# Performance work log

Measured on AMD Instinct MI355X. Metric: run time of the kernel, lower is better.

The kernel has to match this reference:

```python
import jax, jax.numpy as jnp
import numpy as np

DIM = 1024
HEADS = 8
HEAD_DIM = DIM // HEADS
FFN = 4096
B, N = 32, 1024
EPS = 1e-5


def layer_norm(x, g, b):
    mu = jnp.mean(x, axis=-1, keepdims=True)
    var = jnp.mean(jnp.square(x - mu), axis=-1, keepdims=True)
    return (x - mu) * jax.lax.rsqrt(var + EPS) * g + b


def setup_inputs() -> dict:
    key = jax.random.key(0)
    ks = jax.random.split(key, 10)
    s = 0.02
    return {
        "x": jax.random.normal(ks[0], (B, N, DIM), dtype=jnp.float32),
        "haltingscore": jnp.zeros((B, N), dtype=jnp.float32),
        "Wq": jax.random.normal(ks[1], (DIM, DIM), dtype=jnp.float32) * s,
        "Wkv": jax.random.normal(ks[2], (DIM, 2 * DIM), dtype=jnp.float32) * s,
        "Wp": jax.random.normal(ks[3], (DIM, DIM), dtype=jnp.float32) * s,
        "bp": jnp.zeros((DIM,), dtype=jnp.float32),
        "W1": jax.random.normal(ks[4], (DIM, FFN), dtype=jnp.float32) * s,
        "b1": jnp.zeros((FFN,), dtype=jnp.float32),
        "W2": jax.random.normal(ks[5], (FFN, DIM), dtype=jnp.float32) * s,
        "b2": jnp.zeros((DIM,), dtype=jnp.float32),
        "ln1_g": jnp.ones((DIM,), dtype=jnp.float32),
        "ln1_b": jnp.zeros((DIM,), dtype=jnp.float32),
        "ln2_g": jnp.ones((DIM,), dtype=jnp.float32),
        "ln2_b": jnp.zeros((DIM,), dtype=jnp.float32),
    }


def reference(x, haltingscore, Wq, Wkv, Wp, bp, W1, b1, W2, b2,
              ln1_g, ln1_b, ln2_g, ln2_b):
    b, n, c = x.shape
    scale = HEAD_DIM ** -0.5
    # ---- EfficientAttention (explicit QK^T softmax V) ----
    q = (x @ Wq).reshape(b, n, HEADS, HEAD_DIM).transpose(0, 2, 1, 3)  # bhnd
    kv = (x @ Wkv).reshape(b, n, 2, HEADS, HEAD_DIM).transpose(2, 0, 3, 1, 4)
    k, v = kv[0], kv[1]                                               # bhnd
    attn = jax.nn.softmax(jnp.einsum('bhnd,bhmd->bhnm', q, k) * scale, axis=-1)
    o = jnp.einsum('bhnm,bhmd->bhnd', attn, v)
    o = o.transpose(0, 2, 1, 3).reshape(b, n, c)
    o = o @ Wp + bp
    attn_mean = jnp.mean(attn, axis=1)                                # (B, N, N)
    # ---- residual + LN1 ----
    h = layer_norm(x + o, ln1_g, ln1_b)
    # ---- FFN + residual + LN2 ----
    ff = jax.nn.relu(h @ W1 + b1) @ W2 + b2
    out = layer_norm(h + ff, ln2_g, ln2_b)
    # ---- halting score update ----
    a = jax.nn.softmax(jnp.sum(attn_mean, axis=1), axis=-1)           # (B, N)
    halting = haltingscore + a
    return (out, halting, a)
```

## Files before the change

### kernel.cpp

```cpp
#include <hip/hip_runtime.h>
#include <hip/hip_bf16.h>
#include <stdint.h>

#define DIMC 1024
#define HEADS 8
#define HDIM 128
#define FFND 4096
#define BATCH 32
#define SEQ 1024
#define SROWS (BATCH*SEQ)
#define QSTR 3072

typedef unsigned short u16;
typedef short short4v __attribute__((ext_vector_type(4)));
typedef short short8 __attribute__((ext_vector_type(8)));
typedef float f32x4 __attribute__((ext_vector_type(4)));
typedef __bf16 bf16x8 __attribute__((ext_vector_type(8)));

__device__ __forceinline__ u16 f2bf(float f) {
    union { float f; uint32_t u; } x{f};
    uint32_t r = x.u + 0x7FFFu + ((x.u >> 16) & 1u);
    return (u16)(r >> 16);
}
__device__ __forceinline__ float bf2f(u16 h) {
    union { uint32_t u; float f; } x;
    x.u = ((uint32_t)h) << 16;
    return x.f;
}

__device__ __forceinline__ f32x4 mfma16(short8 a, short8 b, f32x4 c) {
    return __builtin_amdgcn_mfma_f32_16x16x32_bf16(
        __builtin_bit_cast(bf16x8, a), __builtin_bit_cast(bf16x8, b), c, 0, 0, 0);
}

__device__ __forceinline__ void gload_lds16(const u16* g, u16* lds) {
    __builtin_amdgcn_global_load_lds(
        (const __attribute__((address_space(1))) uint32_t*)g,
        (__attribute__((address_space(3))) uint32_t*)lds, 16, 0, 0);
}

__global__ __launch_bounds__(256) void k_cast(const float* __restrict__ in,
                                              u16* __restrict__ out, int n4) {
    int i = blockIdx.x * 256 + threadIdx.x;
    if (i < n4) {
        f32x4 v = ((const f32x4*)in)[i];
        uint32_t lo = f2bf(v[0]) | ((uint32_t)f2bf(v[1]) << 16);
        uint32_t hi = f2bf(v[2]) | ((uint32_t)f2bf(v[3]) << 16);
        ((uint2*)out)[i] = make_uint2(lo, hi);
    }
}

__global__ __launch_bounds__(256) void k_transpose_cast(const float* __restrict__ W,
                                                        u16* __restrict__ Wt,
                                                        int K, int N) {
    __shared__ u16 tile[32][33];
    int n0 = blockIdx.x * 32, k0 = blockIdx.y * 32;
    int tx = threadIdx.x, ty = threadIdx.y;
#pragma unroll
    for (int i = 0; i < 32; i += 8)
        tile[ty + i][tx] = f2bf(W[(size_t)(k0 + ty + i) * N + n0 + tx]);
    __syncthreads();
#pragma unroll
    for (int i = 0; i < 32; i += 8)
        Wt[(size_t)(n0 + ty + i) * K + k0 + tx] = tile[tx][ty + i];
}

template<bool OUT_BF16, bool RELU, bool BIAS, bool VSPLIT>
__global__ __launch_bounds__(512, 2) void k_gemm256(const u16* __restrict__ A,
                                                    const u16* __restrict__ Bt,
                                                    const float* __restrict__ bias,
                                                    void* __restrict__ C,
                                                    u16* __restrict__ Vt,
                                                    int M, int N, int K) {
    union Smem {
        struct { u16 A[4][8192]; u16 B[4][8192]; } k;
        u16 ob[64 * 264];
        float of[64 * 268];
        u16 vt[256 * 66];
    };
    __shared__ Smem smem;
    const int tid = threadIdx.x;
    const int lane = tid & 63, wv = tid >> 6;
    const int wm = wv >> 2, wn = wv & 3;
    const int l15 = lane & 15, lg = lane >> 4;
    const int gx = gridDim.x;
    const int nwg = gx * gridDim.y;
    const int id = blockIdx.y * gx + blockIdx.x;
    const int id2 = (id & 7) * (nwg >> 3) + (id >> 3);
    const int row0 = (id2 / gx) << 8, col0 = (id2 % gx) << 8;
    const int NT = K >> 5;

#define STAGE_A(tt) {                                                          \
    int _t = (tt);                                                             \
    _Pragma("unroll")                                                          \
    for (int i = 0; i < 2; ++i) {                                              \
        int blk = wv * 2 + i;                                                  \
        gload_lds16(A + (size_t)(row0 + blk * 16 + l15) * K + _t * 32 + lg * 8,\
                    &smem.k.A[_t & 3][blk * 512]);                             \
    } }
#define STAGE_B(tt) {                                                          \
    int _t = (tt);                                                             \
    _Pragma("unroll")                                                          \
    for (int i = 0; i < 2; ++i) {                                              \
        int blk = wv * 2 + i;                                                  \
        gload_lds16(Bt + (size_t)(col0 + blk * 16 + l15) * K + _t * 32 + lg * 8,\
                    &smem.k.B[_t & 3][blk * 512]);                             \
    } }

    STAGE_A(0); STAGE_B(0);
    STAGE_A(1); STAGE_B(1);
    STAGE_A(2); STAGE_B(2);

    f32x4 acc[8][4] = {};
    for (int t = 0; t < NT; ++t) {
        const int slot = t & 3;
        if (t <= NT - 3)      asm volatile("s_waitcnt vmcnt(8)" ::: "memory");
        else if (t == NT - 2) asm volatile("s_waitcnt vmcnt(4)" ::: "memory");
        else                  asm volatile("s_waitcnt vmcnt(0)" ::: "memory");
        __builtin_amdgcn_s_barrier();
        __builtin_amdgcn_sched_barrier(0);

        const u16* Ab = &smem.k.A[slot][(wm * 8) * 512];
        const u16* Bb = &smem.k.B[slot][(wn * 4) * 512];

        if (t + 3 < NT) STAGE_A(t + 3);
        short8 bf[4], af[4];
#pragma unroll
        for (int n = 0; n < 4; ++n) bf[n] = *(const short8*)(Bb + n * 512 + lane * 8);
#pragma unroll
        for (int m = 0; m < 4; ++m) af[m] = *(const short8*)(Ab + m * 512 + lane * 8);
        __builtin_amdgcn_s_setprio(1);
#pragma unroll
        for (int m = 0; m < 4; ++m)
#pragma unroll
            for (int n = 0; n < 4; ++n)
                acc[m][n] = mfma16(af[m], bf[n], acc[m][n]);
        __builtin_amdgcn_s_setprio(0);

        if (t + 3 < NT) STAGE_B(t + 3);
#pragma unroll
        for (int m = 0; m < 4; ++m) af[m] = *(const short8*)(Ab + (4 + m) * 512 + lane * 8);
        __builtin_amdgcn_s_setprio(1);
#pragma unroll
        for (int m = 0; m < 4; ++m)
#pragma unroll
            for (int n = 0; n < 4; ++n)
                acc[4 + m][n] = mfma16(af[m], bf[n], acc[4 + m][n]);
        __builtin_amdgcn_s_setprio(0);
    }
#undef STAGE_A
#undef STAGE_B

    const bool vpath = VSPLIT && (col0 >= 2048);
    __syncthreads();
#pragma unroll
    for (int s = 0; s < 4; ++s) {
        if (s) __syncthreads();
        if (wm == (s >> 1)) {
            const int mb4 = (s & 1) * 4;
#pragma unroll
            for (int mm = 0; mm < 4; ++mm)
#pragma unroll
                for (int n = 0; n < 4; ++n) {
                    int c = wn * 64 + n * 16 + l15;
                    float bv = BIAS ? bias[col0 + c] : 0.f;
#pragma unroll
                    for (int j = 0; j < 4; ++j) {
                        int lr = mm * 16 + lg * 4 + j;
                        float v = acc[mb4 + mm][n][j] + bv;
                        if (RELU) v = fmaxf(v, 0.f);
                        if (vpath)         smem.vt[c * 66 + lr] = f2bf(v);
                        else if (OUT_BF16) smem.ob[lr * 264 + c] = f2bf(v);
                        else               smem.of[lr * 268 + c] = v;
                    }
                }
        }
        __syncthreads();
        const int gr0 = row0 + s * 64;
        if (vpath) {
            const int bb = gr0 >> 10;
            const int mb = gr0 & 1023;
#pragma unroll
            for (int it = 0; it < 4; ++it) {
                int idx = it * 512 + tid;
                int dc = idx >> 3, mseg = idx & 7;
                int hh = (col0 - 2048 + dc) >> 7;
                int dd = (col0 - 2048 + dc) & 127;
                *(short8*)(Vt + ((size_t)(bb * 8 + hh)) * (HDIM * SEQ)
                              + (size_t)dd * SEQ + mb + mseg * 8) =
                    *(const short8*)(&smem.vt[dc * 66 + mseg * 8]);
            }
        } else if (OUT_BF16) {
#pragma unroll
            for (int it = 0; it < 4; ++it) {
                int idx = it * 512 + tid;
                int r = idx >> 5, seg = idx & 31;
                *(short8*)((u16*)C + (size_t)(gr0 + r) * N + col0 + seg * 8) =
                    *(const short8*)(&smem.ob[r * 264 + seg * 8]);
            }
        } else {
#pragma unroll
            for (int it = 0; it < 8; ++it) {
                int idx = it * 512 + tid;
                int r = idx >> 6, seg = idx & 63;
                *(f32x4*)((float*)C + (size_t)(gr0 + r) * N + col0 + seg * 4) =
                    *(const f32x4*)(&smem.of[r * 268 + seg * 4]);
            }
        }
    }
}

__global__ __launch_bounds__(256, 3) void k_attn(const u16* __restrict__ QKV,
                                                 const u16* __restrict__ Vt,
                                                 u16* __restrict__ O,
                                                 float* __restrict__ csp) {
    __shared__ u16 Kl[2][4096];
    __shared__ u16 Vl[2][4096];
    __shared__ u16 p_lds[4][1280];
    __shared__ float cs[1024];
    const int id = blockIdx.x;
    const int id2 = (id & 7) * 256 + (id >> 3);
    const int qt = id2 & 7, bh = id2 >> 3;
    const int b = bh >> 3, h = bh & 7;
    const int tid = threadIdx.x, lane = tid & 63, wv = tid >> 6;
    const int l15 = lane & 15, lg = lane >> 4;

    for (int i = tid; i < 1024; i += 256) cs[i] = 0.f;

    const int q0 = qt * 128 + wv * 32;
    const u16* qbaseA = QKV + (size_t)(b * SEQ + q0 + l15) * QSTR + h * HDIM + lg * 8;
    const u16* qbaseB = qbaseA + (size_t)16 * QSTR;
    short8 qfA[4], qfB[4];
#pragma unroll
    for (int kk = 0; kk < 4; ++kk) {
        qfA[kk] = *(const short8*)(qbaseA + kk * 32);
        qfB[kk] = *(const short8*)(qbaseB + kk * 32);
    }
    const float CEXP = 0.12751743f;
    const u16* kbase = QKV + (size_t)(b * SEQ) * QSTR + 1024 + h * HDIM;
    const u16* vtb = Vt + (size_t)bh * HDIM * SEQ;

#define STAGE_K(tt) { _Pragma("unroll")                                         \
    for (int i = 0; i < 2; ++i) { int c = wv * 2 + i;                           \
        gload_lds16(kbase + (size_t)((tt) * 32 + (c >> 2) * 16 + l15) * QSTR    \
                    + (c & 3) * 32 + lg * 8, &Kl[(tt) & 1][c * 512]); } }
#define STAGE_V(tt) { _Pragma("unroll")                                         \
    for (int i = 0; i < 2; ++i) { int c = wv * 2 + i;                           \
        gload_lds16(vtb + (size_t)(c * 16 + l15) * SEQ + (tt) * 32 + lg * 8,    \
                    &Vl[(tt) & 1][c * 512]); } }

    STAGE_K(0);
    asm volatile("s_waitcnt vmcnt(0)" ::: "memory");
    __builtin_amdgcn_s_barrier();
    f32x4 rsA = {0.f, 0.f, 0.f, 0.f}, rsB = {0.f, 0.f, 0.f, 0.f};
    for (int t = 0; t < 32; ++t) {
        if (t < 31) STAGE_K(t + 1);
        const u16* Kp = &Kl[t & 1][0];
        f32x4 sA0 = {0.f,0.f,0.f,0.f}, sA1 = {0.f,0.f,0.f,0.f};
        f32x4 sB0 = {0.f,0.f,0.f,0.f}, sB1 = {0.f,0.f,0.f,0.f};
        __builtin_amdgcn_s_setprio(1);
#pragma unroll
        for (int kk = 0; kk < 4; ++kk) {
            short8 b0 = *(const short8*)(Kp + kk * 512 + lane * 8);
            short8 b1 = *(const short8*)(Kp + (4 + kk) * 512 + lane * 8);
            sA0 = mfma16(qfA[kk], b0, sA0);
            sA1 = mfma16(qfA[kk], b1, sA1);
            sB0 = mfma16(qfB[kk], b0, sB0);
            sB1 = mfma16(qfB[kk], b1, sB1);
        }
        __builtin_amdgcn_s_setprio(0);
#pragma unroll
        for (int r = 0; r < 4; ++r) {
            rsA[r] += __builtin_amdgcn_exp2f(sA0[r] * CEXP)
                    + __builtin_amdgcn_exp2f(sA1[r] * CEXP);
            rsB[r] += __builtin_amdgcn_exp2f(sB0[r] * CEXP)
                    + __builtin_amdgcn_exp2f(sB1[r] * CEXP);
        }
        asm volatile("s_waitcnt vmcnt(0)" ::: "memory");
        __builtin_amdgcn_s_barrier();
    }
#pragma unroll
    for (int o = 1; o < 16; o <<= 1)
#pragma unroll
        for (int r = 0; r < 4; ++r) {
            rsA[r] += __shfl_xor(rsA[r], o);
            rsB[r] += __shfl_xor(rsB[r], o);
        }
    f32x4 inv_rsA, inv_rsB;
#pragma unroll
    for (int r = 0; r < 4; ++r) {
        inv_rsA[r] = 1.f / rsA[r];
        inv_rsB[r] = 1.f / rsB[r];
    }

    STAGE_K(0); STAGE_V(0);
    asm volatile("s_waitcnt vmcnt(0)" ::: "memory");
    __builtin_amdgcn_s_barrier();
    f32x4 odA[8] = {}, odB[8] = {};
    u16* pl = &p_lds[wv][0];
    for (int t = 0; t < 32; ++t) {
        const int m0 = t * 32;
        if (t < 31) { STAGE_K(t + 1); STAGE_V(t + 1); }
        const u16* Kp = &Kl[t & 1][0];
        f32x4 sA0 = {0.f,0.f,0.f,0.f}, sA1 = {0.f,0.f,0.f,0.f};
        f32x4 sB0 = {0.f,0.f,0.f,0.f}, sB1 = {0.f,0.f,0.f,0.f};
        __builtin_amdgcn_s_setprio(1);
#pragma unroll
        for (int kk = 0; kk < 4; ++kk) {
            short8 b0 = *(const short8*)(Kp + kk * 512 + lane * 8);
            short8 b1 = *(const short8*)(Kp + (4 + kk) * 512 + lane * 8);
            sA0 = mfma16(qfA[kk], b0, sA0);
            sA1 = mfma16(qfA[kk], b1, sA1);
            sB0 = mfma16(qfB[kk], b0, sB0);
            sB1 = mfma16(qfB[kk], b1, sB1);
        }
        __builtin_amdgcn_s_setprio(0);
        float pA0[4], pA1[4], pB0[4], pB1[4];
#pragma unroll
        for (int r = 0; r < 4; ++r) {
            pA0[r] = __builtin_amdgcn_exp2f(sA0[r] * CEXP) * inv_rsA[r];
            pA1[r] = __builtin_amdgcn_exp2f(sA1[r] * CEXP) * inv_rsA[r];
            pB0[r] = __builtin_amdgcn_exp2f(sB0[r] * CEXP) * inv_rsB[r];
            pB1[r] = __builtin_amdgcn_exp2f(sB1[r] * CEXP) * inv_rsB[r];
        }
        float c0 = pA0[0] + pA0[1] + pA0[2] + pA0[3]
                 + pB0[0] + pB0[1] + pB0[2] + pB0[3];
        float c1 = pA1[0] + pA1[1] + pA1[2] + pA1[3]
                 + pB1[0] + pB1[1] + pB1[2] + pB1[3];
        c0 += __shfl_xor(c0, 16); c0 += __shfl_xor(c0, 32);
        c1 += __shfl_xor(c1, 16); c1 += __shfl_xor(c1, 32);
        if (lane < 16)      atomicAdd(&cs[m0 + lane], c0);
        else if (lane < 32) atomicAdd(&cs[m0 + lane], c1);
#pragma unroll
        for (int r = 0; r < 4; ++r) {
            pl[(lg * 4 + r) * 40 + l15]           = f2bf(pA0[r]);
            pl[(lg * 4 + r) * 40 + 16 + l15]      = f2bf(pA1[r]);
            pl[(16 + lg * 4 + r) * 40 + l15]      = f2bf(pB0[r]);
            pl[(16 + lg * 4 + r) * 40 + 16 + l15] = f2bf(pB1[r]);
        }
        short8 paA = *(const short8*)(pl + l15 * 40 + lg * 8);
        short8 paB = *(const short8*)(pl + (16 + l15) * 40 + lg * 8);
        const u16* Vb_ = &Vl[t & 1][0];
        __builtin_amdgcn_s_setprio(1);
#pragma unroll
        for (int db = 0; db < 8; ++db) {
            short8 vf = *(const short8*)(Vb_ + db * 512 + lane * 8);
            odA[db] = mfma16(paA, vf, odA[db]);
            odB[db] = mfma16(paB, vf, odB[db]);
        }
        __builtin_amdgcn_s_setprio(0);
        asm volatile("s_waitcnt vmcnt(0)" ::: "memory");
        __builtin_amdgcn_s_barrier();
    }
#undef STAGE_K
#undef STAGE_V
    __syncthreads();
    u16* obA = O + (size_t)(b * SEQ + q0 + lg * 4) * DIMC + h * HDIM + l15;
    u16* obB = obA + (size_t)16 * DIMC;
#pragma unroll
    for (int db = 0; db < 8; ++db)
#pragma unroll
        for (int r = 0; r < 4; ++r) {
            obA[(size_t)r * DIMC + db * 16] = f2bf(odA[db][r]);
            obB[(size_t)r * DIMC + db * 16] = f2bf(odB[db][r]);
        }
    for (int m = tid; m < 1024; m += 256)
        csp[((size_t)bh * 8 + qt) * 1024 + m] = cs[m];
}

__global__ __launch_bounds__(256) void k_ln1(const float* __restrict__ xa,
                                             const u16* __restrict__ pj,
                                             const float* __restrict__ g,
                                             const float* __restrict__ bt,
                                             u16* __restrict__ ob) {
    const int row = blockIdx.x;
    const int t = threadIdx.x, lane = t & 63, wv = t >> 6;
    f32x4 va = ((const f32x4*)(xa + (size_t)row * DIMC))[t];
    short4v hv = ((const short4v*)(pj + (size_t)row * DIMC))[t];
    f32x4 s;
#pragma unroll
    for (int j = 0; j < 4; ++j) s[j] = va[j] + bf2f((u16)hv[j]);
    float sum = s[0] + s[1] + s[2] + s[3];
    float sq = s[0]*s[0] + s[1]*s[1] + s[2]*s[2] + s[3]*s[3];
#pragma unroll
    for (int o = 1; o < 64; o <<= 1) { sum += __shfl_xor(sum, o); sq += __shfl_xor(sq, o); }
    __shared__ float red[8];
    if (lane == 0) { red[wv] = sum; red[4 + wv] = sq; }
    __syncthreads();
    sum = red[0] + red[1] + red[2] + red[3];
    sq  = red[4] + red[5] + red[6] + red[7];
    float mu = sum * (1.f / DIMC);
    float rstd = rsqrtf(sq * (1.f / DIMC) - mu * mu + 1e-5f);
    f32x4 gg = ((const f32x4*)g)[t];
    f32x4 bb = ((const f32x4*)bt)[t];
    uint32_t lo, hi;
    float o0 = (s[0] - mu) * rstd * gg[0] + bb[0];
    float o1 = (s[1] - mu) * rstd * gg[1] + bb[1];
    float o2 = (s[2] - mu) * rstd * gg[2] + bb[2];
    float o3 = (s[3] - mu) * rstd * gg[3] + bb[3];
    lo = f2bf(o0) | ((uint32_t)f2bf(o1) << 16);
    hi = f2bf(o2) | ((uint32_t)f2bf(o3) << 16);
    ((uint2*)(ob + (size_t)row * DIMC))[t] = make_uint2(lo, hi);
}

__global__ __launch_bounds__(256) void k_ln2(const u16* __restrict__ xa,
                                             const u16* __restrict__ f2,
                                             const float* __restrict__ g,
                                             const float* __restrict__ bt,
                                             float* __restrict__ of) {
    const int row = blockIdx.x;
    const int t = threadIdx.x, lane = t & 63, wv = t >> 6;
    short4v hv = ((const short4v*)(xa + (size_t)row * DIMC))[t];
    short4v fv = ((const short4v*)(f2 + (size_t)row * DIMC))[t];
    f32x4 s;
#pragma unroll
    for (int j = 0; j < 4; ++j) s[j] = bf2f((u16)hv[j]) + bf2f((u16)fv[j]);
    float sum = s[0] + s[1] + s[2] + s[3];
    float sq = s[0]*s[0] + s[1]*s[1] + s[2]*s[2] + s[3]*s[3];
#pragma unroll
    for (int o = 1; o < 64; o <<= 1) { sum += __shfl_xor(sum, o); sq += __shfl_xor(sq, o); }
    __shared__ float red[8];
    if (lane == 0) { red[wv] = sum; red[4 + wv] = sq; }
    __syncthreads();
    sum = red[0] + red[1] + red[2] + red[3];
    sq  = red[4] + red[5] + red[6] + red[7];
    float mu = sum * (1.f / DIMC);
    float rstd = rsqrtf(sq * (1.f / DIMC) - mu * mu + 1e-5f);
    f32x4 gg = ((const f32x4*)g)[t];
    f32x4 bb = ((const f32x4*)bt)[t];
    f32x4 o4;
#pragma unroll
    for (int j = 0; j < 4; ++j) o4[j] = (s[j] - mu) * rstd * gg[j] + bb[j];
    ((f32x4*)(of + (size_t)row * DIMC))[t] = o4;
}

__global__ __launch_bounds__(256) void k_halt(const float* __restrict__ csp,
                                              const float* __restrict__ hs,
                                              float* __restrict__ halt_out,
                                              float* __restrict__ a_out) {
    const int b = blockIdx.x, t = threadIdx.x, lane = t & 63, wv = t >> 6;
    const float* base = csp + (size_t)b * 65536;
    float acc[4] = {0.f, 0.f, 0.f, 0.f};
    for (int s2 = 0; s2 < 64; ++s2) {
#pragma unroll
        for (int j = 0; j < 4; ++j) acc[j] += base[(size_t)s2 * 1024 + j * 256 + t];
    }
    float mx = -1e30f;
#pragma unroll
    for (int j = 0; j < 4; ++j) { acc[j] *= 0.125f; mx = fmaxf(mx, acc[j]); }
#pragma unroll
    for (int o = 1; o < 64; o <<= 1) mx = fmaxf(mx, __shfl_xor(mx, o));
    __shared__ float red[8];
    if (lane == 0) red[wv] = mx;
    __syncthreads();
    mx = fmaxf(fmaxf(red[0], red[1]), fmaxf(red[2], red[3]));
    float e[4]; float sum = 0.f;
#pragma unroll
    for (int j = 0; j < 4; ++j) { e[j] = __expf(acc[j] - mx); sum += e[j]; }
#pragma unroll
    for (int o = 1; o < 64; o <<= 1) sum += __shfl_xor(sum, o);
    if (lane == 0) red[4 + wv] = sum;
    __syncthreads();
    sum = red[4] + red[5] + red[6] + red[7];
    float inv = 1.f / sum;
#pragma unroll
    for (int j = 0; j < 4; ++j) {
        int m = j * 256 + t;
        float a = e[j] * inv;
        a_out[b * SEQ + m] = a;
        halt_out[b * SEQ + m] = hs[b * SEQ + m] + a;
    }
}

extern "C" void kernel_launch(void* const* d_in, const int* in_sizes, int n_in,
                              void* d_out, int out_size, void* d_ws, size_t ws_size,
                              hipStream_t stream) {
    (void)in_sizes; (void)n_in; (void)out_size; (void)ws_size;
    const float* x   = (const float*)d_in[0];
    const float* hs  = (const float*)d_in[1];
    const float* Wq  = (const float*)d_in[2];
    const float* Wkv = (const float*)d_in[3];
    const float* Wp  = (const float*)d_in[4];
    const float* bp  = (const float*)d_in[5];
    const float* W1  = (const float*)d_in[6];
    const float* b1  = (const float*)d_in[7];
    const float* W2  = (const float*)d_in[8];
    const float* b2  = (const float*)d_in[9];
    const float* g1  = (const float*)d_in[10];
    const float* be1 = (const float*)d_in[11];
    const float* g2  = (const float*)d_in[12];
    const float* be2 = (const float*)d_in[13];

    float* out = (float*)d_out;
    float* halt_out = out + (size_t)SROWS * DIMC;
    float* a_out = halt_out + SROWS;

    char* w = (char*)d_ws;
    const size_t MB = 1024 * 1024;
    u16*  xb    = (u16*)(w);
    u16*  qkv   = (u16*)(w + 64 * MB);
    u16*  Vt    = (u16*)(w + 256 * MB);
    u16*  WqkvT = (u16*)(w + 320 * MB);
    u16*  WpT   = (u16*)(w + 326 * MB);
    u16*  W1T   = (u16*)(w + 328 * MB);
    u16*  W2T   = (u16*)(w + 336 * MB);
    float* csp  = (float*)(w + 344 * MB);
    u16*  o_b   = (u16*)(w);
    u16*  projb = (u16*)(w + 64 * MB);
    u16*  hb    = (u16*)(w);
    u16*  ff1   = (u16*)(w + 64 * MB);
    u16*  ff2b  = (u16*)(w + 192 * MB);

    dim3 tb(32, 8);
    k_cast<<<SROWS * DIMC / 4 / 256, 256, 0, stream>>>(x, xb, SROWS * DIMC / 4);
    k_transpose_cast<<<dim3(DIMC / 32, DIMC / 32), tb, 0, stream>>>(Wq, WqkvT, DIMC, DIMC);
    k_transpose_cast<<<dim3(2 * DIMC / 32, DIMC / 32), tb, 0, stream>>>(
        Wkv, WqkvT + (size_t)DIMC * DIMC, DIMC, 2 * DIMC);
    k_transpose_cast<<<dim3(DIMC / 32, DIMC / 32), tb, 0, stream>>>(Wp, WpT, DIMC, DIMC);
    k_transpose_cast<<<dim3(FFND / 32, DIMC / 32), tb, 0, stream>>>(W1, W1T, DIMC, FFND);
    k_transpose_cast<<<dim3(DIMC / 32, FFND / 32), tb, 0, stream>>>(W2, W2T, FFND, DIMC);
    k_gemm256<true, false, false, true><<<dim3(QSTR / 256, SROWS / 256), 512, 0, stream>>>(
        xb, WqkvT, nullptr, qkv, Vt, SROWS, QSTR, DIMC);
    k_attn<<<2048, 256, 0, stream>>>(qkv, Vt, o_b, csp);
    k_gemm256<true, false, true, false><<<dim3(DIMC / 256, SROWS / 256), 512, 0, stream>>>(
        o_b, WpT, bp, projb, nullptr, SROWS, DIMC, DIMC);
    k_ln1<<<SROWS, 256, 0, stream>>>(x, projb, g1, be1, hb);
    for (int c = 0; c < 2; ++c) {
        const size_t ro = (size_t)c * 16384;
        k_gemm256<true, true, true, false><<<dim3(FFND / 256, 16384 / 256), 512, 0, stream>>>(
            hb + ro * DIMC, W1T, b1, ff1, nullptr, 16384, FFND, DIMC);
        k_gemm256<true, false, true, false><<<dim3(DIMC / 256, 16384 / 256), 512, 0, stream>>>(
            ff1, W2T, b2, ff2b, nullptr, 16384, DIMC, FFND);
        k_ln2<<<16384, 256, 0, stream>>>(hb + ro * DIMC, ff2b, g2, be2, out + ro * DIMC);
    }
    k_halt<<<BATCH, 256, 0, stream>>>(csp, hs, halt_out, a_out);
}
```

Baseline: 1.472 ms.

## Transpose QK MFMA operands and build P fragments in registers via cross-lane shuffles

Swaps the MFMA operand order so S^T is computed, giving each lane a column of scores. The P→bf16 fragment is then assembled in registers with v_cvt_pk_bf16_f32 and xor shuffles, removing the per-wave LDS round trip for P. Column sums for the attention mean now use DPP row-rotate reductions. The row-sum pass loads 64-key tiles through a union-shared LDS buffer, halving its barrier count. This trades LDS traffic and barriers for extra shuffle and select instructions, and the fragment-permutation correctness is delicate.

Result: no change. 1.445 ms (-1.8%).

```diff
diff --git a/kernel.cpp b/kernel.cpp
--- a/kernel.cpp
+++ b/kernel.cpp
@@ -37,6 +37,36 @@
     __builtin_amdgcn_global_load_lds(
         (const __attribute__((address_space(1))) uint32_t*)g,
         (__attribute__((address_space(3))) uint32_t*)lds, 16, 0, 0);
+}
+
+#define DPP_RORADD(x, ctrl) do {                                               \
+    int _t = __builtin_amdgcn_mov_dpp(__builtin_bit_cast(int, (x)), (ctrl),    \
+                                      0xf, 0xf, true);                         \
+    (x) += __builtin_bit_cast(float, _t); } while (0)
+
+__device__ __forceinline__ short8 p2frag(f32x4 p0, f32x4 p1, int lane) {
+    uint32_t a, b, c, d;
+    asm("v_cvt_pk_bf16_f32 %0, %1, %2" : "=v"(a) : "v"(p0[0]), "v"(p0[1]));
+    asm("v_cvt_pk_bf16_f32 %0, %1, %2" : "=v"(b) : "v"(p0[2]), "v"(p0[3]));
+    asm("v_cvt_pk_bf16_f32 %0, %1, %2" : "=v"(c) : "v"(p1[0]), "v"(p1[1]));
+    asm("v_cvt_pk_bf16_f32 %0, %1, %2" : "=v"(d) : "v"(p1[2]), "v"(p1[3]));
+    uint32_t ax = (uint32_t)__shfl_xor((int)a, 32);
+    uint32_t bx = (uint32_t)__shfl_xor((int)b, 32);
+    uint32_t cx = (uint32_t)__shfl_xor((int)c, 32);
+    uint32_t dx = (uint32_t)__shfl_xor((int)d, 32);
+    const bool up = (lane & 32) != 0;
+    uint32_t P = up ? cx : a, Q = up ? c : ax;
+    uint32_t R = up ? dx : b, S = up ? d : bx;
+    uint32_t Px = (uint32_t)__shfl_xor((int)P, 16);
+    uint32_t Qx = (uint32_t)__shfl_xor((int)Q, 16);
+    uint32_t Rx = (uint32_t)__shfl_xor((int)R, 16);
+    uint32_t Sx = (uint32_t)__shfl_xor((int)S, 16);
+    const bool odd = (lane & 16) != 0;
+    uint32_t w0 = odd ? Qx : P,  w1 = odd ? Sx : R;
+    uint32_t w2 = odd ? Q  : Px, w3 = odd ? S  : Rx;
+    union { uint32_t w[4]; short8 s; } u;
+    u.w[0] = w0; u.w[1] = w1; u.w[2] = w2; u.w[3] = w3;
+    return u.s;
 }
 
 __global__ __launch_bounds__(256) void k_cast(const float* __restrict__ in,
@@ -214,9 +244,11 @@
                                                  const u16* __restrict__ Vt,
                                                  u16* __restrict__ O,
                                                  float* __restrict__ csp) {
-    __shared__ u16 Kl[2][4096];
-    __shared__ u16 Vl[2][4096];
-    __shared__ u16 p_lds[4][1280];
+    union Sm {
+        u16 K2[2][8192];
+        struct { u16 Kl[2][4096]; u16 Vl[2][4096]; } pb;
+    };
+    __shared__ Sm sm;
     __shared__ float cs[1024];
     const int id = blockIdx.x;
     const int id2 = (id & 7) * 256 + (id >> 3);
@@ -240,107 +272,115 @@
     const u16* kbase = QKV + (size_t)(b * SEQ) * QSTR + 1024 + h * HDIM;
     const u16* vtb = Vt + (size_t)bh * HDIM * SEQ;
 
+#define STAGE_K2(tt) { _Pragma("unroll")                                        \
+    for (int i = 0; i < 4; ++i) {                                               \
+        gload_lds16(kbase + (size_t)((tt) * 64 + wv * 16 + l15) * QSTR          \
+                    + i * 32 + lg * 8, &sm.K2[(tt) & 1][(wv * 4 + i) * 512]); } }
 #define STAGE_K(tt) { _Pragma("unroll")                                         \
     for (int i = 0; i < 2; ++i) { int c = wv * 2 + i;                           \
         gload_lds16(kbase + (size_t)((tt) * 32 + (c >> 2) * 16 + l15) * QSTR    \
-                    + (c & 3) * 32 + lg * 8, &Kl[(tt) & 1][c * 512]); } }
+                    + (c & 3) * 32 + lg * 8, &sm.pb.Kl[(tt) & 1][c * 512]); } }
 #define STAGE_V(tt) { _Pragma("unroll")                                         \
     for (int i = 0; i < 2; ++i) { int c = wv * 2 + i;                           \
         gload_lds16(vtb + (size_t)(c * 16 + l15) * SEQ + (tt) * 32 + lg * 8,    \
-                    &Vl[(tt) & 1][c * 512]); } }
-
-    STAGE_K(0);
+                    &sm.pb.Vl[(tt) & 1][c * 512]); } }
+
+    STAGE_K2(0);
     asm volatile("s_waitcnt vmcnt(0)" ::: "memory");
     __builtin_amdgcn_s_barrier();
-    f32x4 rsA = {0.f, 0.f, 0.f, 0.f}, rsB = {0.f, 0.f, 0.f, 0.f};
-    for (int t = 0; t < 32; ++t) {
-        if (t < 31) STAGE_K(t + 1);
-        const u16* Kp = &Kl[t & 1][0];
-        f32x4 sA0 = {0.f,0.f,0.f,0.f}, sA1 = {0.f,0.f,0.f,0.f};
-        f32x4 sB0 = {0.f,0.f,0.f,0.f}, sB1 = {0.f,0.f,0.f,0.f};
+    f32x4 rsA4 = {0.f, 0.f, 0.f, 0.f}, rsB4 = {0.f, 0.f, 0.f, 0.f};
+    for (int t = 0; t < 16; ++t) {
+        if (t < 15) STAGE_K2(t + 1);
+        const u16* Kp = &sm.K2[t & 1][0];
         __builtin_amdgcn_s_setprio(1);
 #pragma unroll
-        for (int kk = 0; kk < 4; ++kk) {
-            short8 b0 = *(const short8*)(Kp + kk * 512 + lane * 8);
-            short8 b1 = *(const short8*)(Kp + (4 + kk) * 512 + lane * 8);
-            sA0 = mfma16(qfA[kk], b0, sA0);
-            sA1 = mfma16(qfA[kk], b1, sA1);
-            sB0 = mfma16(qfB[kk], b0, sB0);
-            sB1 = mfma16(qfB[kk], b1, sB1);
+        for (int j = 0; j < 4; j += 2) {
+            f32x4 s0 = {0.f,0.f,0.f,0.f}, s1 = {0.f,0.f,0.f,0.f};
+            f32x4 s2 = {0.f,0.f,0.f,0.f}, s3 = {0.f,0.f,0.f,0.f};
+#pragma unroll
+            for (int kk = 0; kk < 4; ++kk) {
+                short8 k0 = *(const short8*)(Kp + (j * 4 + kk) * 512 + lane * 8);
+                short8 k1 = *(const short8*)(Kp + ((j + 1) * 4 + kk) * 512 + lane * 8);
+                s0 = mfma16(k0, qfA[kk], s0);
+                s1 = mfma16(k0, qfB[kk], s1);
+                s2 = mfma16(k1, qfA[kk], s2);
+                s3 = mfma16(k1, qfB[kk], s3);
+            }
+#pragma unroll
+            for (int r = 0; r < 4; ++r) {
+                rsA4[r] += __builtin_amdgcn_exp2f(s0[r] * CEXP)
+                         + __builtin_amdgcn_exp2f(s2[r] * CEXP);
+                rsB4[r] += __builtin_amdgcn_exp2f(s1[r] * CEXP)
+                         + __builtin_amdgcn_exp2f(s3[r] * CEXP);
+            }
         }
         __builtin_amdgcn_s_setprio(0);
-#pragma unroll
-        for (int r = 0; r < 4; ++r) {
-            rsA[r] += __builtin_amdgcn_exp2f(sA0[r] * CEXP)
-                    + __builtin_amdgcn_exp2f(sA1[r] * CEXP);
-            rsB[r] += __builtin_amdgcn_exp2f(sB0[r] * CEXP)
-                    + __builtin_amdgcn_exp2f(sB1[r] * CEXP);
-        }
         asm volatile("s_waitcnt vmcnt(0)" ::: "memory");
         __builtin_amdgcn_s_barrier();
     }
-#pragma unroll
-    for (int o = 1; o < 16; o <<= 1)
-#pragma unroll
-        for (int r = 0; r < 4; ++r) {
-            rsA[r] += __shfl_xor(rsA[r], o);
-            rsB[r] += __shfl_xor(rsB[r], o);
-        }
-    f32x4 inv_rsA, inv_rsB;
-#pragma unroll
-    for (int r = 0; r < 4; ++r) {
-        inv_rsA[r] = 1.f / rsA[r];
-        inv_rsB[r] = 1.f / rsB[r];
-    }
+    float rsA = (rsA4[0] + rsA4[1]) + (rsA4[2] + rsA4[3]);
+    float rsB = (rsB4[0] + rsB4[1]) + (rsB4[2] + rsB4[3]);
+    rsA += __shfl_xor(rsA, 16); rsA += __shfl_xor(rsA, 32);
+    rsB += __shfl_xor(rsB, 16); rsB += __shfl_xor(rsB, 32);
+    const float invA = 1.f / rsA, invB = 1.f / rsB;
 
     STAGE_K(0); STAGE_V(0);
     asm volatile("s_waitcnt vmcnt(0)" ::: "memory");
     __builtin_amdgcn_s_barrier();
     f32x4 odA[8] = {}, odB[8] = {};
-    u16* pl = &p_lds[wv][0];
     for (int t = 0; t < 32; ++t) {
         const int m0 = t * 32;
         if (t < 31) { STAGE_K(t + 1); STAGE_V(t + 1); }
-        const u16* Kp = &Kl[t & 1][0];
+        const u16* Kp = &sm.pb.Kl[t & 1][0];
         f32x4 sA0 = {0.f,0.f,0.f,0.f}, sA1 = {0.f,0.f,0.f,0.f};
         f32x4 sB0 = {0.f,0.f,0.f,0.f}, sB1 = {0.f,0.f,0.f,0.f};
         __builtin_amdgcn_s_setprio(1);
 #pragma unroll
         for (int kk = 0; kk < 4; ++kk) {
-            short8 b0 = *(const short8*)(Kp + kk * 512 + lane * 8);
-            short8 b1 = *(const short8*)(Kp + (4 + kk) * 512 + lane * 8);
-            sA0 = mfma16(qfA[kk], b0, sA0);
-            sA1 = mfma16(qfA[kk], b1, sA1);
-            sB0 = mfma16(qfB[kk], b0, sB0);
-            sB1 = mfma16(qfB[kk], b1, sB1);
+            short8 k0 = *(const short8*)(Kp + kk * 512 + lane * 8);
+            short8 k1 = *(const short8*)(Kp + (4 + kk) * 512 + lane * 8);
+            sA0 = mfma16(k0, qfA[kk], sA0);
+            sA1 = mfma16(k1, qfA[kk], sA1);
+            sB0 = mfma16(k0, qfB[kk], sB0);
+            sB1 = mfma16(k1, qfB[kk], sB1);
         }
         __builtin_amdgcn_s_setprio(0);
-        float pA0[4], pA1[4], pB0[4], pB1[4];
+        f32x4 pA0, pA1, pB0, pB1;
 #pragma unroll
         for (int r = 0; r < 4; ++r) {
-            pA0[r] = __builtin_amdgcn_exp2f(sA0[r] * CEXP) * inv_rsA[r];
-            pA1[r] = __builtin_amdgcn_exp2f(sA1[r] * CEXP) * inv_rsA[r];
-            pB0[r] = __builtin_amdgcn_exp2f(sB0[r] * CEXP) * inv_rsB[r];
-            pB1[r] = __builtin_amdgcn_exp2f(sB1[r] * CEXP) * inv_rsB[r];
-        }
-        float c0 = pA0[0] + pA0[1] + pA0[2] + pA0[3]
-                 + pB0[0] + pB0[1] + pB0[2] + pB0[3];
-        float c1 = pA1[0] + pA1[1] + pA1[2] + pA1[3]
-                 + pB1[0] + pB1[1] + pB1[2] + pB1[3];
-        c0 += __shfl_xor(c0, 16); c0 += __shfl_xor(c0, 32);
-        c1 += __shfl_xor(c1, 16); c1 += __shfl_xor(c1, 32);
-        if (lane < 16)      atomicAdd(&cs[m0 + lane], c0);
-        else if (lane < 32) atomicAdd(&cs[m0 + lane], c1);
+            pA0[r] = __builtin_amdgcn_exp2f(sA0[r] * CEXP) * invA;
+            pA1[r] = __builtin_amdgcn_exp2f(sA1[r] * CEXP) * invA;
+            pB0[r] = __builtin_amdgcn_exp2f(sB0[r] * CEXP) * invB;
+            pB1[r] = __builtin_amdgcn_exp2f(sB1[r] * CEXP) * invB;
+        }
+        float csv[8];
 #pragma unroll
         for (int r = 0; r < 4; ++r) {
-            pl[(lg * 4 + r) * 40 + l15]           = f2bf(pA0[r]);
-            pl[(lg * 4 + r) * 40 + 16 + l15]      = f2bf(pA1[r]);
-            pl[(16 + lg * 4 + r) * 40 + l15]      = f2bf(pB0[r]);
-            pl[(16 + lg * 4 + r) * 40 + 16 + l15] = f2bf(pB1[r]);
-        }
-        short8 paA = *(const short8*)(pl + l15 * 40 + lg * 8);
-        short8 paB = *(const short8*)(pl + (16 + l15) * 40 + lg * 8);
-        const u16* Vb_ = &Vl[t & 1][0];
+            csv[r]     = pA0[r] + pB0[r];
+            csv[4 + r] = pA1[r] + pB1[r];
+        }
+#pragma unroll
+        for (int j2 = 0; j2 < 8; ++j2) {
+            DPP_RORADD(csv[j2], 0x128);
+            DPP_RORADD(csv[j2], 0x124);
+            DPP_RORADD(csv[j2], 0x122);
+            DPP_RORADD(csv[j2], 0x121);
+        }
+        float cval = csv[0];
+        cval = (l15 == 1) ? csv[1] : cval;
+        cval = (l15 == 2) ? csv[2] : cval;
+        cval = (l15 == 3) ? csv[3] : cval;
+        cval = (l15 == 4) ? csv[4] : cval;
+        cval = (l15 == 5) ? csv[5] : cval;
+        cval = (l15 == 6) ? csv[6] : cval;
+        cval = (l15 == 7) ? csv[7] : cval;
+        if (l15 < 8) {
+            int mw = (l15 < 4) ? (lg * 4 + l15) : (16 + lg * 4 + (l15 - 4));
+            atomicAdd(&cs[m0 + mw], cval);
+        }
+        short8 paA = p2frag(pA0, pA1, lane);
+        short8 paB = p2frag(pB0, pB1, lane);
+        const u16* Vb_ = &sm.pb.Vl[t & 1][0];
         __builtin_amdgcn_s_setprio(1);
 #pragma unroll
         for (int db = 0; db < 8; ++db) {
@@ -352,6 +392,7 @@
         asm volatile("s_waitcnt vmcnt(0)" ::: "memory");
         __builtin_amdgcn_s_barrier();
     }
+#undef STAGE_K2
 #undef STAGE_K
 #undef STAGE_V
     __syncthreads();
```
